# Kernel tuning notes

Measured on AMD Instinct MI355X. Metric: run time of the kernel, lower is better.

The kernel has to match this reference:

```python
import jax, jax.numpy as jnp
import numpy as np


def soft_threshold24(w):
    """2:4 soft thresholding along the last dim (groups of 4):
    keep top-2 magnitudes per group, subtract the 2nd-smallest magnitude
    (largest pruned value) from kept elements: sign(w)*relu(|w|-t)."""
    shape = w.shape
    g = w.reshape(-1, 4)
    mag = jnp.abs(g)
    s = jnp.sort(mag, axis=-1)          # ascending: [s0,s1,s2,s3]
    t = s[:, 1:2]                        # threshold = 2nd smallest magnitude
    out = jnp.sign(g) * jnp.maximum(mag - t, 0.0)
    return out.reshape(shape)


def fp8_mm(a, b):
    # fake_fp8_mm: cast operands to fp16, accumulate in fp32
    return jnp.matmul(a.astype(jnp.float16), b.astype(jnp.float16),
                      preferred_element_type=jnp.float32)


def _init_scale(w):
    ws = soft_threshold24(w)
    return jnp.sum(w * ws) / jnp.sum(ws * ws)


def setup_inputs() -> dict:
    key = jax.random.key(0)
    k1, k2, k3 = jax.random.split(key, 3)
    in_f, out_f, rank = 4096, 4096, 64
    B, S = 4, 2048
    x = jax.random.normal(k1, (B, S, in_f), dtype=jnp.float32)
    # kaiming_uniform_(a=sqrt(5)) -> U(-1/sqrt(fan_in), 1/sqrt(fan_in))
    b_in = 1.0 / np.sqrt(in_f)
    b_out = 1.0 / np.sqrt(rank)
    weight_in = jax.random.uniform(k2, (rank, in_f), minval=-b_in, maxval=b_in, dtype=jnp.float32)
    weight_out = jax.random.uniform(k3, (out_f, rank), minval=-b_out, maxval=b_out, dtype=jnp.float32)
    bias = jnp.zeros((out_f,), dtype=jnp.float32)
    scale_in = _init_scale(weight_in).astype(jnp.float32)
    scale_out = _init_scale(weight_out).astype(jnp.float32)
    return {"x": x, "weight_in": weight_in, "weight_out": weight_out,
            "bias": bias, "scale_in": scale_in, "scale_out": scale_out}


def reference(x, weight_in, weight_out, bias, scale_in, scale_out):
    rank = weight_in.shape[0]
    scaling = 1.0 / rank  # alpha / rank, alpha = 1.0
    sw_in = soft_threshold24(weight_in) * scale_in    # (rank, in_f)
    sw_out = soft_threshold24(weight_out) * scale_out  # (out_f, rank)
    B, S, in_f = x.shape
    xp = fp8_mm(x.reshape(-1, in_f), sw_in.T)          # (B*S, rank) fp32
    out = fp8_mm(xp, sw_out.T) + bias                   # (B*S, out_f)
    return out.reshape(B, S, -1) * scaling
```

## Files before the change

### kernel.cpp

```cpp
#include <hip/hip_runtime.h>

typedef _Float16 half8 __attribute__((ext_vector_type(8)));
typedef float f32x4 __attribute__((ext_vector_type(4)));

#define IN_F 4096
#define OUT_F 4096
#define RANK 64
#define M_TOT 8192
#define KCHUNK 1024
#define NKC (IN_F / KCHUNK)

__device__ __forceinline__ half8 thresh8(const float* __restrict__ p, float scale) {
    half8 h;
    #pragma unroll
    for (int g = 0; g < 2; ++g) {
        f32x4 v = *(const f32x4*)(p + 4 * g);
        float m0 = fabsf(v[0]), m1 = fabsf(v[1]), m2 = fabsf(v[2]), m3 = fabsf(v[3]);
        float lo1 = fminf(m0, m1), hi1 = fmaxf(m0, m1);
        float lo2 = fminf(m2, m3), hi2 = fmaxf(m2, m3);
        float t = fminf(fmaxf(lo1, lo2), fminf(hi1, hi2));
        h[4 * g + 0] = (_Float16)(copysignf(fmaxf(m0 - t, 0.0f), v[0]) * scale);
        h[4 * g + 1] = (_Float16)(copysignf(fmaxf(m1 - t, 0.0f), v[1]) * scale);
        h[4 * g + 2] = (_Float16)(copysignf(fmaxf(m2 - t, 0.0f), v[2]) * scale);
        h[4 * g + 3] = (_Float16)(copysignf(fmaxf(m3 - t, 0.0f), v[3]) * scale);
    }
    return h;
}

__global__ __launch_bounds__(256) void prep_kernel(
    const float* __restrict__ w_in, const float* __restrict__ w_out,
    const float* __restrict__ s_in_p, const float* __restrict__ s_out_p,
    _Float16* __restrict__ sw_in, _Float16* __restrict__ sw_out)
{
    const int tid = blockIdx.x * 256 + threadIdx.x;
    const int HALF = RANK * IN_F / 8;
    const float* src; _Float16* dst; float sc; int g;
    if (tid < HALF) { src = w_in;  dst = sw_in;  sc = *s_in_p;  g = tid; }
    else            { src = w_out; dst = sw_out; sc = *s_out_p; g = tid - HALF; }
    half8 h = thresh8(src + (size_t)g * 8, sc);
    *(half8*)(dst + (size_t)g * 8) = h;
}

__global__ __launch_bounds__(256) void loro_main(
    const float* __restrict__ x, const _Float16* __restrict__ sw_in,
    const _Float16* __restrict__ sw_out, const float* __restrict__ bias,
    float* __restrict__ out)
{
    __shared__ _Float16 xh[2][16][KCHUNK];
    __shared__ _Float16 xpl[16][RANK];

    const int t    = threadIdx.x;
    const int wave = t >> 6;
    const int lane = t & 63;
    const int row  = lane & 15;
    const int kg   = lane >> 4;
    const int m0   = blockIdx.x * 16;

    const int sr  = t >> 7;
    const int skb = t & 127;

    f32x4 ra[8], rb[8];

    auto issue = [&](int kc) {
        #pragma unroll
        for (int i = 0; i < 8; ++i) {
            const float* src = x + (size_t)(m0 + i * 2 + sr) * IN_F + kc + skb * 8;
            ra[i] = *(const f32x4*)src;
            rb[i] = *(const f32x4*)(src + 4);
        }
    };
    auto cstore = [&](int buf) {
        #pragma unroll
        for (int i = 0; i < 8; ++i) {
            const int r = i * 2 + sr;
            half8 h;
            #pragma unroll
            for (int j = 0; j < 4; ++j) {
                h[j]     = (_Float16)ra[i][j];
                h[j + 4] = (_Float16)rb[i][j];
            }
            *(half8*)&xh[buf][r][(skb ^ (r & 7)) << 3] = h;
        }
    };

    const _Float16* wr = sw_in + (size_t)(wave * 16 + row) * IN_F + kg * 8;
    f32x4 acc1 = {0.f, 0.f, 0.f, 0.f};

    issue(0);
    cstore(0);
    __syncthreads();
    int cur = 0;
    for (int kci = 0; kci < NKC; ++kci) {
        if (kci + 1 < NKC) issue((kci + 1) * KCHUNK);
        const int kc = kci * KCHUNK;
        #pragma unroll 4
        for (int k0 = 0; k0 < KCHUNK; k0 += 64) {
            const int kb = (k0 >> 3) + kg;
            half8 alo = *(const half8*)&xh[cur][row][(kb       ^ (row & 7)) << 3];
            half8 ahi = *(const half8*)&xh[cur][row][((kb + 4) ^ (row & 7)) << 3];
            half8 blo = *(const half8*)(wr + kc + k0);
            half8 bhi = *(const half8*)(wr + kc + k0 + 32);
            acc1 = __builtin_amdgcn_mfma_f32_16x16x32_f16(alo, blo, acc1, 0, 0, 0);
            acc1 = __builtin_amdgcn_mfma_f32_16x16x32_f16(ahi, bhi, acc1, 0, 0, 0);
        }
        if (kci + 1 < NKC) cstore(cur ^ 1);
        __syncthreads();
        cur ^= 1;
    }

    #pragma unroll
    for (int r = 0; r < 4; ++r)
        xpl[kg * 4 + r][wave * 16 + row] = (_Float16)acc1[r];
    __syncthreads();

    const half8 a_lo = *(const half8*)&xpl[row][kg * 8];
    const half8 a_hi = *(const half8*)&xpl[row][kg * 8 + 32];
    const float scaling = 1.0f / 64.0f;

    for (int c = 0; c < 16; ++c) {
        f32x4 acc[4] = {{0.f,0.f,0.f,0.f},{0.f,0.f,0.f,0.f},
                        {0.f,0.f,0.f,0.f},{0.f,0.f,0.f,0.f}};
        #pragma unroll
        for (int nt = 0; nt < 4; ++nt) {
            const _Float16* wp = sw_out
                + (size_t)(c * 256 + wave * 64 + nt * 16 + row) * RANK + kg * 8;
            half8 blo = *(const half8*)wp;
            half8 bhi = *(const half8*)(wp + 32);
            acc[nt] = __builtin_amdgcn_mfma_f32_16x16x32_f16(a_lo, blo, acc[nt], 0, 0, 0);
            acc[nt] = __builtin_amdgcn_mfma_f32_16x16x32_f16(a_hi, bhi, acc[nt], 0, 0, 0);
        }
        #pragma unroll
        for (int nt = 0; nt < 4; ++nt) {
            const int col = c * 256 + wave * 64 + nt * 16 + row;
            const float b = bias[col];
            #pragma unroll
            for (int r = 0; r < 4; ++r)
                out[(size_t)(m0 + kg * 4 + r) * OUT_F + col] = (acc[nt][r] + b) * scaling;
        }
    }
}

__global__ __launch_bounds__(256) void loro_fallback(
    const float* __restrict__ x, const float* __restrict__ w_in,
    const float* __restrict__ w_out, const float* __restrict__ bias,
    const float* __restrict__ s_in_p, const float* __restrict__ s_out_p,
    float* __restrict__ out)
{
    __shared__ _Float16 xh[16][KCHUNK];
    __shared__ _Float16 xpl[16][RANK];

    const int t    = threadIdx.x;
    const int wave = t >> 6;
    const int lane = t & 63;
    const int row  = lane & 15;
    const int kg   = lane >> 4;
    const int m0   = blockIdx.x * 16;
    const float s_in  = *s_in_p;
    const float s_out = *s_out_p;

    f32x4 acc1 = {0.f, 0.f, 0.f, 0.f};
    const float* wr = w_in + (size_t)(wave * 16 + row) * IN_F + kg * 8;

    for (int kc = 0; kc < IN_F; kc += KCHUNK) {
        __syncthreads();
        #pragma unroll
        for (int i = 0; i < 8; ++i) {
            const int f  = i * 2048 + t * 8;
            const int r  = f >> 10;
            const int cl = f & (KCHUNK - 1);
            const float* src = x + (size_t)(m0 + r) * IN_F + kc + cl;
            f32x4 a = *(const f32x4*)src;
            f32x4 b = *(const f32x4*)(src + 4);
            #pragma unroll
            for (int j = 0; j < 4; ++j) {
                xh[r][cl + j]     = (_Float16)a[j];
                xh[r][cl + 4 + j] = (_Float16)b[j];
            }
        }
        __syncthreads();

        #pragma unroll 4
        for (int k0 = 0; k0 < KCHUNK; k0 += 64) {
            half8 alo = *(const half8*)&xh[row][k0 + kg * 8];
            half8 ahi = *(const half8*)&xh[row][k0 + kg * 8 + 32];
            half8 blo = thresh8(wr + kc + k0,      s_in);
            half8 bhi = thresh8(wr + kc + k0 + 32, s_in);
            acc1 = __builtin_amdgcn_mfma_f32_16x16x32_f16(alo, blo, acc1, 0, 0, 0);
            acc1 = __builtin_amdgcn_mfma_f32_16x16x32_f16(ahi, bhi, acc1, 0, 0, 0);
        }
    }

    #pragma unroll
    for (int r = 0; r < 4; ++r)
        xpl[kg * 4 + r][wave * 16 + row] = (_Float16)acc1[r];
    __syncthreads();

    const half8 a_lo = *(const half8*)&xpl[row][kg * 8];
    const half8 a_hi = *(const half8*)&xpl[row][kg * 8 + 32];
    const float scaling = 1.0f / 64.0f;

    for (int c = 0; c < 16; ++c) {
        f32x4 acc[4] = {{0.f,0.f,0.f,0.f},{0.f,0.f,0.f,0.f},
                        {0.f,0.f,0.f,0.f},{0.f,0.f,0.f,0.f}};
        #pragma unroll
        for (int nt = 0; nt < 4; ++nt) {
            const float* wp = w_out
                + (size_t)(c * 256 + wave * 64 + nt * 16 + row) * RANK + kg * 8;
            half8 blo = thresh8(wp,      s_out);
            half8 bhi = thresh8(wp + 32, s_out);
            acc[nt] = __builtin_amdgcn_mfma_f32_16x16x32_f16(a_lo, blo, acc[nt], 0, 0, 0);
            acc[nt] = __builtin_amdgcn_mfma_f32_16x16x32_f16(a_hi, bhi, acc[nt], 0, 0, 0);
        }
        #pragma unroll
        for (int nt = 0; nt < 4; ++nt) {
            const int col = c * 256 + wave * 64 + nt * 16 + row;
            const float b = bias[col];
            #pragma unroll
            for (int r = 0; r < 4; ++r)
                out[(size_t)(m0 + kg * 4 + r) * OUT_F + col] = (acc[nt][r] + b) * scaling;
        }
    }
}

extern "C" void kernel_launch(void* const* d_in, const int* in_sizes, int n_in,
                              void* d_out, int out_size, void* d_ws, size_t ws_size,
                              hipStream_t stream) {
    (void)in_sizes; (void)n_in; (void)out_size;
    const float* x     = (const float*)d_in[0];
    const float* w_in  = (const float*)d_in[1];
    const float* w_out = (const float*)d_in[2];
    const float* bias  = (const float*)d_in[3];
    const float* s_in  = (const float*)d_in[4];
    const float* s_out = (const float*)d_in[5];

    const size_t need = (size_t)(RANK * IN_F + OUT_F * RANK) * sizeof(_Float16);
    if (d_ws != nullptr && ws_size >= need) {
        _Float16* sw_in  = (_Float16*)d_ws;
        _Float16* sw_out = sw_in + (size_t)RANK * IN_F;
        prep_kernel<<<(RANK * IN_F + OUT_F * RANK) / 8 / 256, 256, 0, stream>>>(
            w_in, w_out, s_in, s_out, sw_in, sw_out);
        loro_main<<<M_TOT / 16, 256, 0, stream>>>(x, sw_in, sw_out, bias, (float*)d_out);
    } else {
        loro_fallback<<<M_TOT / 16, 256, 0, stream>>>(
            x, w_in, w_out, bias, s_in, s_out, (float*)d_out);
    }
}
```

Before: 92.01 us.

## Split fused kernel into split-K first GEMM and wide second GEMM kernels

Replaces the single fused kernel, which uses 512 blocks, with two kernels. The first GEMM is split four ways along K into 2048 blocks that write fp32 partial sums to workspace. The second GEMM then reduces those partials and computes the output over 2048 blocks, each covering 1024 columns. The aim is more parallelism and better latency hiding on the large GPU. The cost is an extra kernel launch and an 8 MB round trip of partials through global memory, and the new path only runs when the workspace is large enough.

```diff
diff --git a/kernel.cpp b/kernel.cpp
--- a/kernel.cpp
+++ b/kernel.cpp
@@ -9,6 +9,7 @@
 #define M_TOT 8192
 #define KCHUNK 1024
 #define NKC (IN_F / KCHUNK)
+#define KSPLIT 4
 
 __device__ __forceinline__ half8 thresh8(const float* __restrict__ p, float scale) {
     half8 h;
@@ -41,7 +42,125 @@
     *(half8*)(dst + (size_t)g * 8) = h;
 }
 
-__global__ __launch_bounds__(256) void loro_main(
+__global__ __launch_bounds__(256) void gemm1_ks(
+    const float* __restrict__ x, const _Float16* __restrict__ sw_in,
+    float* __restrict__ xpp)
+{
+    __shared__ _Float16 xh[16][KCHUNK];
+    __shared__ float red[KSPLIT][16][RANK];
+
+    const int t    = threadIdx.x;
+    const int wave = t >> 6;
+    const int lane = t & 63;
+    const int row  = lane & 15;
+    const int kg   = lane >> 4;
+    const int mt   = blockIdx.x >> 2;
+    const int ks   = blockIdx.x & 3;
+    const int m0   = mt * 16;
+    const int kbase = ks * KCHUNK;
+
+    {
+        const int sr  = t >> 7;
+        const int skb = t & 127;
+        #pragma unroll
+        for (int i = 0; i < 8; ++i) {
+            const int r = i * 2 + sr;
+            const float* src = x + (size_t)(m0 + r) * IN_F + kbase + skb * 8;
+            f32x4 a = *(const f32x4*)src;
+            f32x4 b = *(const f32x4*)(src + 4);
+            half8 h;
+            #pragma unroll
+            for (int j = 0; j < 4; ++j) { h[j] = (_Float16)a[j]; h[j + 4] = (_Float16)b[j]; }
+            *(half8*)&xh[r][(skb ^ (r & 7)) << 3] = h;
+        }
+    }
+    __syncthreads();
+
+    f32x4 acc[4] = {{0.f,0.f,0.f,0.f},{0.f,0.f,0.f,0.f},
+                    {0.f,0.f,0.f,0.f},{0.f,0.f,0.f,0.f}};
+    const _Float16* wbase = sw_in + kbase + wave * 256 + kg * 8;
+    #pragma unroll
+    for (int s = 0; s < 4; ++s) {
+        const int kb = wave * 32 + s * 8 + kg;
+        half8 alo = *(const half8*)&xh[row][(kb       ^ (row & 7)) << 3];
+        half8 ahi = *(const half8*)&xh[row][((kb + 4) ^ (row & 7)) << 3];
+        #pragma unroll
+        for (int nt = 0; nt < 4; ++nt) {
+            const _Float16* wp = wbase + (size_t)(nt * 16 + row) * IN_F + s * 64;
+            half8 blo = *(const half8*)wp;
+            half8 bhi = *(const half8*)(wp + 32);
+            acc[nt] = __builtin_amdgcn_mfma_f32_16x16x32_f16(alo, blo, acc[nt], 0, 0, 0);
+            acc[nt] = __builtin_amdgcn_mfma_f32_16x16x32_f16(ahi, bhi, acc[nt], 0, 0, 0);
+        }
+    }
+
+    #pragma unroll
+    for (int nt = 0; nt < 4; ++nt)
+        #pragma unroll
+        for (int r = 0; r < 4; ++r)
+            red[wave][kg * 4 + r][nt * 16 + row] = acc[nt][r];
+    __syncthreads();
+
+    for (int i = t; i < 16 * RANK; i += 256) {
+        const int m = i >> 6, n = i & 63;
+        float s = (red[0][m][n] + red[1][m][n]) + (red[2][m][n] + red[3][m][n]);
+        xpp[((size_t)ks * M_TOT + m0 + m) * RANK + n] = s;
+    }
+}
+
+__global__ __launch_bounds__(256) void gemm2_big(
+    const float* __restrict__ xpp, const _Float16* __restrict__ sw_out,
+    const float* __restrict__ bias, float* __restrict__ out)
+{
+    __shared__ _Float16 xpl[16][RANK + 8];
+
+    const int t    = threadIdx.x;
+    const int wave = t >> 6;
+    const int lane = t & 63;
+    const int row  = lane & 15;
+    const int kg   = lane >> 4;
+    const int mt   = blockIdx.x >> 2;
+    const int nc   = blockIdx.x & 3;
+    const int m0   = mt * 16;
+
+    for (int i = t; i < 16 * RANK; i += 256) {
+        const int m = i >> 6, n = i & 63;
+        const size_t base = (size_t)(m0 + m) * RANK + n;
+        const size_t S = (size_t)M_TOT * RANK;
+        float s = (xpp[base] + xpp[S + base]) + (xpp[2 * S + base] + xpp[3 * S + base]);
+        xpl[m][n] = (_Float16)s;
+    }
+    __syncthreads();
+
+    const half8 a_lo = *(const half8*)&xpl[row][kg * 8];
+    const half8 a_hi = *(const half8*)&xpl[row][kg * 8 + 32];
+    const float scaling = 1.0f / 64.0f;
+
+    #pragma unroll
+    for (int c = 0; c < 4; ++c) {
+        const int cg = nc * 1024 + wave * 256 + c * 64;
+        f32x4 acc[4] = {{0.f,0.f,0.f,0.f},{0.f,0.f,0.f,0.f},
+                        {0.f,0.f,0.f,0.f},{0.f,0.f,0.f,0.f}};
+        #pragma unroll
+        for (int nt = 0; nt < 4; ++nt) {
+            const _Float16* wp = sw_out + (size_t)(cg + nt * 16 + row) * RANK + kg * 8;
+            half8 blo = *(const half8*)wp;
+            half8 bhi = *(const half8*)(wp + 32);
+            acc[nt] = __builtin_amdgcn_mfma_f32_16x16x32_f16(a_lo, blo, acc[nt], 0, 0, 0);
+            acc[nt] = __builtin_amdgcn_mfma_f32_16x16x32_f16(a_hi, bhi, acc[nt], 0, 0, 0);
+        }
+        #pragma unroll
+        for (int nt = 0; nt < 4; ++nt) {
+            const int col = cg + nt * 16 + row;
+            const float b = bias[col];
+            #pragma unroll
+            for (int r = 0; r < 4; ++r)
+                out[(size_t)(m0 + kg * 4 + r) * OUT_F + col] = (acc[nt][r] + b) * scaling;
+        }
+    }
+}
+
+__global__ __launch_bounds__(256) void loro_fused16(
     const float* __restrict__ x, const _Float16* __restrict__ sw_in,
     const _Float16* __restrict__ sw_out, const float* __restrict__ bias,
     float* __restrict__ out)
@@ -233,13 +352,24 @@
     const float* s_in  = (const float*)d_in[4];
     const float* s_out = (const float*)d_in[5];
 
-    const size_t need = (size_t)(RANK * IN_F + OUT_F * RANK) * sizeof(_Float16);
-    if (d_ws != nullptr && ws_size >= need) {
+    const size_t need_sw   = (size_t)(RANK * IN_F + OUT_F * RANK) * sizeof(_Float16);
+    const size_t need_full = need_sw + (size_t)KSPLIT * M_TOT * RANK * sizeof(float);
+
+    if (d_ws != nullptr && ws_size >= need_full) {
+        _Float16* sw_in  = (_Float16*)d_ws;
+        _Float16* sw_out = sw_in + (size_t)RANK * IN_F;
+        float*    xpp    = (float*)((char*)d_ws + need_sw);
+        prep_kernel<<<(RANK * IN_F + OUT_F * RANK) / 8 / 256, 256, 0, stream>>>(
+            w_in, w_out, s_in, s_out, sw_in, sw_out);
+        gemm1_ks<<<(M_TOT / 16) * KSPLIT, 256, 0, stream>>>(x, sw_in, xpp);
+        gemm2_big<<<(M_TOT / 16) * (OUT_F / 1024), 256, 0, stream>>>(
+            xpp, sw_out, bias, (float*)d_out);
+    } else if (d_ws != nullptr && ws_size >= need_sw) {
         _Float16* sw_in  = (_Float16*)d_ws;
         _Float16* sw_out = sw_in + (size_t)RANK * IN_F;
         prep_kernel<<<(RANK * IN_F + OUT_F * RANK) / 8 / 256, 256, 0, stream>>>(
             w_in, w_out, s_in, s_out, sw_in, sw_out);
-        loro_main<<<M_TOT / 16, 256, 0, stream>>>(x, sw_in, sw_out, bias, (float*)d_out);
+        loro_fused16<<<M_TOT / 16, 256, 0, stream>>>(x, sw_in, sw_out, bias, (float*)d_out);
     } else {
         loro_fallback<<<M_TOT / 16, 256, 0, stream>>>(
             x, w_in, w_out, bias, s_in, s_out, (float*)d_out);
```

Measured after the change: 99.00 us. +7.6%, slower.
